# Kernel optimization log

Hardware: AMD Instinct MI355X
Metric: run time of the kernel (lower is better)

Reference implementation:

```python
import jax, jax.numpy as jnp
import numpy as np

B, C, H, W = 512, 3, 32, 32
N = 50000
D = C * H * W  # 3072


def setup_inputs() -> dict:
    key = jax.random.key(0)
    k1, k2, k3 = jax.random.split(key, 3)
    x = jax.random.normal(k1, (B, C, H, W), dtype=jnp.float32)
    # per-sample noise levels, strictly positive
    sigma = jax.random.uniform(k2, (B,), dtype=jnp.float32, minval=0.5, maxval=2.0)
    # reference dataset, normalized images in [-1, 1], flattened to (N, D)
    y = jax.random.uniform(k3, (N, D), dtype=jnp.float32, minval=-1.0, maxval=1.0)
    return {"x": x, "sigma": sigma, "y": y}


def reference(x, sigma, y):
    Bb, Cc, Hh, Ww = x.shape
    xf = x.astype(jnp.float32).reshape(Bb, Cc * Hh * Ww)          # (B, D)
    s = sigma.astype(jnp.float32).reshape(-1, 1)                  # (B, 1)
    # squared euclidean distance via the GEMM expansion (matches cdist(p=2)**2)
    x2 = jnp.sum(xf * xf, axis=1, keepdims=True)                  # (B, 1)
    y2 = jnp.sum(y * y, axis=1)[None, :]                          # (1, N)
    d2 = jnp.maximum(x2 + y2 - 2.0 * (xf @ y.T), 0.0)             # (B, N)
    logits = -d2 / (2.0 * s * s)                                  # (B, N)
    prob = jax.nn.softmax(logits, axis=1)                         # (B, N)
    denoised = prob @ y                                           # (B, D)
    return denoised.reshape(Bb, Cc, Hh, Ww)
```

## Files before the change

kernel.cpp:

```cpp
#include <hip/hip_runtime.h>


typedef __attribute__((ext_vector_type(4))) float f32x4;
typedef __attribute__((ext_vector_type(4))) int i32x4;
typedef __attribute__((ext_vector_type(4))) char c8x4;
typedef __attribute__((ext_vector_type(16))) char c8x16;
typedef __attribute__((ext_vector_type(4))) unsigned short u16x4;
typedef __attribute__((ext_vector_type(8))) unsigned short u16x8;
typedef __attribute__((ext_vector_type(8))) __bf16 bf16x8;

#define NREAL 50000
#define NP    50176
#define DD    3072
#define BB    512

#define WAIT0  asm volatile("s_waitcnt vmcnt(0)" ::: "memory")
#define VM2    asm volatile("s_waitcnt vmcnt(2)" ::: "memory")
#define LGKM0  asm volatile("s_waitcnt lgkmcnt(0)" ::: "memory")
#define BAR    __builtin_amdgcn_s_barrier()
#define SCHED0 __builtin_amdgcn_sched_barrier(0)

#define SX (6.0f / 127.0f)
#define SY (1.0f / 127.0f)

__device__ __forceinline__ unsigned short f32_bf16_rne(float f) {
  unsigned int u = __float_as_uint(f);
  unsigned int r = 0x7FFFu + ((u >> 16) & 1u);
  return (unsigned short)((u + r) >> 16);
}
__device__ __forceinline__ void gload16(const void* g, void* l) {
  __builtin_amdgcn_global_load_lds(
      (const __attribute__((address_space(1))) void*)g,
      (__attribute__((address_space(3))) void*)l, 16, 0, 0);
}
__device__ __forceinline__ bf16x8 ldsldb(const unsigned short* p) {
  return __builtin_bit_cast(bf16x8, *(const u16x8*)p);
}
__device__ __forceinline__ i32x4 ldsld4(const char* p) {
  return *(const i32x4*)p;
}
__device__ __forceinline__ char q8(float f, float sc) {
  float an = rintf(f * sc);
  an = fminf(127.f, fmaxf(-127.f, an));
  return (char)(int)an;
}

__global__ __launch_bounds__(256) void zero_kernel(f32x4* p) {
  p[(size_t)blockIdx.x * 256 + threadIdx.x] = (f32x4){0.f, 0.f, 0.f, 0.f};
}

__global__ __launch_bounds__(256) void init_kernel(int* rowmin, float* rowsum) {
  const int i = blockIdx.x * 256 + threadIdx.x;
  if (i < BB) { rowmin[i] = 0x7F800000; rowsum[i] = 0.f; }
}

__global__ __launch_bounds__(256) void prep_x_kernel(
    const float* __restrict__ x, const float* __restrict__ sigma,
    char* __restrict__ ax, char* __restrict__ bx,
    float* __restrict__ x2, float* __restrict__ inv2s2) {
  const int b = blockIdx.x, t = threadIdx.x;
  const f32x4* xr = (const f32x4*)(x + (size_t)b * DD);
  float ssq = 0.f;
#pragma unroll
  for (int i = 0; i < 3; ++i) {
    const int idx = i * 256 + t;
    f32x4 v = xr[idx];
    c8x4 a, bb;
#pragma unroll
    for (int j = 0; j < 4; ++j) {
      float f = v[j];
      ssq += f * f;
      char av = q8(f, 127.0f / 6.0f);
      a[j] = av;
      float r = f - (float)(int)av * SX;
      bb[j] = q8(r, 254.0f * 127.0f / 6.0f);
    }
    *(c8x4*)(ax + (size_t)b * DD + idx * 4) = a;
    *(c8x4*)(bx + (size_t)b * DD + idx * 4) = bb;
  }
  __shared__ float red[4];
#pragma unroll
  for (int off = 32; off > 0; off >>= 1) ssq += __shfl_xor(ssq, off);
  if ((t & 63) == 0) red[t >> 6] = ssq;
  __syncthreads();
  if (t == 0) {
    x2[b] = red[0] + red[1] + red[2] + red[3];
    float s = sigma[b];
    inv2s2[b] = 1.0f / (2.0f * s * s);
  }
}

__global__ __launch_bounds__(256) void quant_y_kernel(
    const float* __restrict__ y, char* __restrict__ ay, char* __restrict__ by,
    float* __restrict__ y2) {
  const int n = blockIdx.x, t = threadIdx.x;
  if (n >= NREAL) {
    c8x4 z = {0, 0, 0, 0};
#pragma unroll
    for (int i = 0; i < 3; ++i) {
      const int idx = i * 256 + t;
      *(c8x4*)(ay + (size_t)n * DD + idx * 4) = z;
      *(c8x4*)(by + (size_t)n * DD + idx * 4) = z;
    }
    if (t == 0) y2[n] = 0.f;
    return;
  }
  const f32x4* yr = (const f32x4*)(y + (size_t)n * DD);
  float ssq = 0.f;
#pragma unroll
  for (int i = 0; i < 3; ++i) {
    const int idx = i * 256 + t;
    f32x4 v = yr[idx];
    c8x4 a, bb;
#pragma unroll
    for (int j = 0; j < 4; ++j) {
      float f = v[j];
      ssq += f * f;
      char av = q8(f, 127.0f);
      a[j] = av;
      float r2 = f - (float)(int)av * SY;
      bb[j] = q8(r2, 254.0f * 127.0f);
    }
    *(c8x4*)(ay + (size_t)n * DD + idx * 4) = a;
    *(c8x4*)(by + (size_t)n * DD + idx * 4) = bb;
  }
  __shared__ float red[4];
#pragma unroll
  for (int off = 32; off > 0; off >>= 1) ssq += __shfl_xor(ssq, off);
  if ((t & 63) == 0) red[t >> 6] = ssq;
  __syncthreads();
  if (t == 0) y2[n] = red[0] + red[1] + red[2] + red[3];
}

__global__ __launch_bounds__(256) void tr_y_kernel(
    const char* __restrict__ ay, const char* __restrict__ by,
    unsigned short* __restrict__ yT) {
  const int bn = blockIdx.x % 784, bd = blockIdx.x / 784;
  const int n0 = bn * 64, d0 = bd * 64;
  __shared__ unsigned short T[64][66];
  const int t = threadIdx.x;
  const int r = t >> 2, cc = (t & 3) * 16;
  c8x16 a = *(const c8x16*)(ay + (size_t)(n0 + r) * DD + d0 + cc);
  c8x16 b = *(const c8x16*)(by + (size_t)(n0 + r) * DD + d0 + cc);
#pragma unroll
  for (int j = 0; j < 16; ++j) {
    float f = (float)((int)a[j] * 254 + (int)b[j]) * (SY / 254.0f);
    T[r][cc + j] = f32_bf16_rne(f);
  }
  __syncthreads();
  const int dr = t >> 2;
#pragma unroll
  for (int k = 0; k < 2; ++k) {
    const int nb = ((t & 3) * 2 + k) * 8;
    u16x8 o;
#pragma unroll
    for (int j = 0; j < 8; ++j) o[j] = T[nb + j][dr];
    *(u16x8*)(yT + (size_t)(d0 + dr) * NP + n0 + nb) = o;
  }
}

__global__ __launch_bounds__(256, 2) void qk_kernel(
    const char* __restrict__ ay, const char* __restrict__ by,
    const char* __restrict__ ax, const char* __restrict__ bx,
    const float* __restrict__ x2, const float* __restrict__ inv2s2,
    const float* __restrict__ y2, float* __restrict__ S, int* __restrict__ rowmin) {
  const int orig = blockIdx.x;
  const int virt = (orig & 7) * 196 + (orig >> 3);
  const int mt = virt & 3, nt = virt >> 2;
  const int m0 = mt * 128, n0 = nt * 128;
  const int t = threadIdx.x, lane = t & 63, w = t >> 6;
  const int wm = w >> 1, wn = w & 1;
  const int l15 = lane & 15;
  const int cs = ((lane >> 4) ^ ((l15 >> 1) & 3)) * 16;

  __shared__ __align__(16) char L[32768];

  i32x4 acc1[4][4] = {};
  i32x4 acc2[4][4] = {};

  const int srow = t >> 2;
  const int sc = ((t & 3) ^ ((t >> 3) & 3)) * 16;
  const int sdst = t * 16;

  const char* pax0 = ax + (size_t)(m0 + srow) * DD + sc;
  const char* pax1 = ax + (size_t)(m0 + srow + 64) * DD + sc;
  const char* pbx0 = bx + (size_t)(m0 + srow) * DD + sc;
  const char* pbx1 = bx + (size_t)(m0 + srow + 64) * DD + sc;
  const char* pay0 = ay + (size_t)(n0 + srow) * DD + sc;
  const char* pay1 = ay + (size_t)(n0 + srow + 64) * DD + sc;
  const char* pby0 = by + (size_t)(n0 + srow) * DD + sc;
  const char* pby1 = by + (size_t)(n0 + srow + 64) * DD + sc;

  auto STAGE = [&]() {
    gload16(pax0, L + sdst);
    gload16(pax1, L + 4096 + sdst);
    gload16(pbx0, L + 8192 + sdst);
    gload16(pbx1, L + 12288 + sdst);
    gload16(pay0, L + 16384 + sdst);
    gload16(pay1, L + 20480 + sdst);
    gload16(pby0, L + 24576 + sdst);
    gload16(pby1, L + 28672 + sdst);
    pax0 += 64; pax1 += 64; pbx0 += 64; pbx1 += 64;
    pay0 += 64; pay1 += 64; pby0 += 64; pby1 += 64;
  };
  auto COMPUTE = [&]() {
    i32x4 axf[4], bxf[4], ayf[4], byf[4];
#pragma unroll
    for (int nf = 0; nf < 4; ++nf) {
      const int row = wn * 64 + nf * 16 + l15;
      ayf[nf] = ldsld4(L + 16384 + row * 64 + cs);
      byf[nf] = ldsld4(L + 24576 + row * 64 + cs);
    }
#pragma unroll
    for (int mf = 0; mf < 4; ++mf) {
      const int row = wm * 64 + mf * 16 + l15;
      axf[mf] = ldsld4(L + row * 64 + cs);
      bxf[mf] = ldsld4(L + 8192 + row * 64 + cs);
    }
    __builtin_amdgcn_s_setprio(1);
#pragma unroll
    for (int mf = 0; mf < 4; ++mf)
#pragma unroll
      for (int nf = 0; nf < 4; ++nf) {
        acc1[mf][nf] = __builtin_amdgcn_mfma_i32_16x16x64_i8(axf[mf], ayf[nf], acc1[mf][nf], 0, 0, 0);
        acc2[mf][nf] = __builtin_amdgcn_mfma_i32_16x16x64_i8(axf[mf], byf[nf], acc2[mf][nf], 0, 0, 0);
        acc2[mf][nf] = __builtin_amdgcn_mfma_i32_16x16x64_i8(bxf[mf], ayf[nf], acc2[mf][nf], 0, 0, 0);
      }
    __builtin_amdgcn_s_setprio(0);
  };

  STAGE();
  for (int k = 0; k < 48; ++k) {
    __syncthreads();
    COMPUTE();
    __syncthreads();
    if (k < 47) STAGE();
  }

  const float C1 = 6.0f / 16129.0f;
  const float C2 = C1 / 254.0f;
  float rmv[4][4];
#pragma unroll
  for (int mf = 0; mf < 4; ++mf)
#pragma unroll
    for (int i = 0; i < 4; ++i) rmv[mf][i] = 3.0e38f;

#pragma unroll
  for (int nf = 0; nf < 4; ++nf) {
    const int col = n0 + wn * 64 + nf * 16 + l15;
    const bool ok = (col < NREAL);
    const float yy = ok ? y2[col] : 0.f;
#pragma unroll
    for (int mf = 0; mf < 4; ++mf) {
#pragma unroll
      for (int i = 0; i < 4; ++i) {
        const int row = m0 + wm * 64 + mf * 16 + ((lane >> 4) * 4) + i;
        float v = 3.0e38f;
        if (ok) {
          float dot = C1 * (float)acc1[mf][nf][i] + C2 * (float)acc2[mf][nf][i];
          float d2 = fmaxf(x2[row] + yy - 2.0f * dot, 0.0f);
          v = d2 * inv2s2[row];
          rmv[mf][i] = fminf(rmv[mf][i], v);
        }
        S[(size_t)row * NP + col] = v;
      }
    }
  }
#pragma unroll
  for (int mf = 0; mf < 4; ++mf)
#pragma unroll
    for (int i = 0; i < 4; ++i) {
      float v = rmv[mf][i];
#pragma unroll
      for (int o = 1; o < 16; o <<= 1) v = fminf(v, __shfl_xor(v, o));
      rmv[mf][i] = v;
    }
  if (l15 == 0) {
#pragma unroll
    for (int mf = 0; mf < 4; ++mf)
#pragma unroll
      for (int i = 0; i < 4; ++i) {
        const int row = m0 + wm * 64 + mf * 16 + ((lane >> 4) * 4) + i;
        atomicMin(rowmin + row, __float_as_int(rmv[mf][i]));
      }
  }
}

__global__ __launch_bounds__(256) void softmax_kernel(
    const float* __restrict__ S, const int* __restrict__ rowmin,
    unsigned short* __restrict__ P, float* __restrict__ rowsum) {
  const int bid = blockIdx.x;
  const int b = bid / 7, c = bid % 7;
  const int t = threadIdx.x;
  const f32x4* row = (const f32x4*)(S + (size_t)b * NP);
  const float rm = __int_as_float(rowmin[b]);
  unsigned short* pr = P + (size_t)b * NP;
  float sum = 0.f;
  const int base = c * 1792;
#pragma unroll
  for (int i = 0; i < 7; ++i) {
    const int e = base + i * 256 + t;
    f32x4 v = row[e];
    float e0 = __expf(rm - v[0]), e1 = __expf(rm - v[1]);
    float e2 = __expf(rm - v[2]), e3 = __expf(rm - v[3]);
    sum += e0 + e1 + e2 + e3;
    u16x4 o;
    o[0] = f32_bf16_rne(e0); o[1] = f32_bf16_rne(e1);
    o[2] = f32_bf16_rne(e2); o[3] = f32_bf16_rne(e3);
    *(u16x4*)(pr + (size_t)e * 4) = o;
  }
#pragma unroll
  for (int off = 32; off > 0; off >>= 1) sum += __shfl_xor(sum, off);
  __shared__ float red[4];
  if ((t & 63) == 0) red[t >> 6] = sum;
  __syncthreads();
  if (t == 0) atomicAdd(rowsum + b, red[0] + red[1] + red[2] + red[3]);
}

__global__ __launch_bounds__(512, 2) void pv_kernel(
    const unsigned short* __restrict__ yT, const unsigned short* __restrict__ P,
    const float* __restrict__ rowsum, float* __restrict__ out) {
  const int orig = blockIdx.x;
  const int virt = (orig & 7) * 96 + (orig >> 3);
  const int sp = virt / 24;
  const int r24 = virt % 24;
  const int dt = r24 >> 1, mt = r24 & 1;
  const int m0 = mt * 256, d0 = dt * 256;
  const int k0t = sp * 24 + (sp < 16 ? sp : 16);
  const int NT = 24 + (sp < 16 ? 1 : 0);

  const int t = threadIdx.x;
  const int lane = t & 63, w = t >> 6;
  const int wm = w >> 2, wn = w & 3;
  const int l15 = lane & 15;
  const int h3 = (l15 >> 1) & 7;
  const int cs0 = ((lane >> 4) ^ h3) * 8;
  const int cs1 = ((4 + (lane >> 4)) ^ h3) * 8;

  __shared__ __align__(16) unsigned short L[2][2][16384];

  f32x4 acc[8][4] = {};

  const int srow8 = t >> 3;
  const int sc = ((t & 7) ^ ((t >> 4) & 7)) * 8;
  const int sdst = t * 8;

  const size_t kbeg = (size_t)k0t * 64;
  const unsigned short* pA[4];
  pA[0] = P + (size_t)(m0 + srow8) * NP + kbeg + sc;
  pA[1] = P + (size_t)(m0 + srow8 + 128) * NP + kbeg + sc;
  pA[2] = P + (size_t)(m0 + srow8 + 64) * NP + kbeg + sc;
  pA[3] = P + (size_t)(m0 + srow8 + 192) * NP + kbeg + sc;
  const unsigned short* pB[4];
#pragma unroll
  for (int r = 0; r < 4; ++r)
    pB[r] = yT + (size_t)(d0 + srow8 + r * 64) * NP + kbeg + sc;

  auto SB01 = [&](int b) {
    gload16(pB[0], &L[b][1][sdst]); gload16(pB[1], &L[b][1][sdst + 4096]);
    pB[0] += 64; pB[1] += 64;
  };
  auto SB23 = [&](int b) {
    gload16(pB[2], &L[b][1][sdst + 8192]); gload16(pB[3], &L[b][1][sdst + 12288]);
    pB[2] += 64; pB[3] += 64;
  };
  auto SA01 = [&](int b) {
    gload16(pA[0], &L[b][0][sdst]); gload16(pA[1], &L[b][0][sdst + 4096]);
    pA[0] += 64; pA[1] += 64;
  };
  auto SA23 = [&](int b) {
    gload16(pA[2], &L[b][0][sdst + 8192]); gload16(pA[3], &L[b][0][sdst + 12288]);
    pA[2] += 64; pA[3] += 64;
  };

  bf16x8 a[4], bv[4];
  auto RA = [&](int b, int mh, int cs) {
#pragma unroll
    for (int m4 = 0; m4 < 4; ++m4)
      a[m4] = ldsldb(&L[b][0][(mh * 128 + wm * 64 + m4 * 16 + l15) * 64 + cs]);
  };
  auto RB = [&](int b, int cs) {
#pragma unroll
    for (int nf = 0; nf < 4; ++nf)
      bv[nf] = ldsldb(&L[b][1][(wn * 64 + nf * 16 + l15) * 64 + cs]);
  };
  auto MF = [&](int mh) {
    __builtin_amdgcn_s_setprio(1);
#pragma unroll
    for (int m4 = 0; m4 < 4; ++m4)
#pragma unroll
      for (int nf = 0; nf < 4; ++nf)
        acc[mh * 4 + m4][nf] = __builtin_amdgcn_mfma_f32_16x16x32_bf16(
            a[m4], bv[nf], acc[mh * 4 + m4][nf], 0, 0, 0);
    __builtin_amdgcn_s_setprio(0);
  };

  SB01(0); SB23(0); SA01(0); SA23(0);
  WAIT0; BAR;

  for (int k = 0; k < NT - 1; ++k) {
    const int b = k & 1, nb = b ^ 1;
    RB(b, cs0); RA(b, 0, cs0);
    SB01(nb);
    BAR; LGKM0; SCHED0;
    MF(0);
    VM2;
    BAR;
    RA(b, 1, cs0);
    SB23(nb);
    BAR; LGKM0; SCHED0;
    MF(1);
    BAR;
    RB(b, cs1); RA(b, 0, cs1);
    SA01(nb);
    BAR; LGKM0; SCHED0;
    MF(0);
    BAR;
    RA(b, 1, cs1);
    SA23(nb);
    BAR; LGKM0; SCHED0;
    MF(1);
    VM2;
    BAR;
  }
  {
    const int b = (NT - 1) & 1;
    RB(b, cs0); RA(b, 0, cs0);
    BAR; LGKM0; SCHED0;
    MF(0);
    WAIT0;
    BAR;
    RA(b, 1, cs0);
    LGKM0; SCHED0;
    MF(1);
    RB(b, cs1); RA(b, 0, cs1);
    LGKM0; SCHED0;
    MF(0);
    RA(b, 1, cs1);
    LGKM0; SCHED0;
    MF(1);
  }

#pragma unroll
  for (int mi = 0; mi < 8; ++mi)
#pragma unroll
    for (int i = 0; i < 4; ++i) {
      const int row = m0 + wm * 128 + mi * 16 + ((lane >> 4) * 4) + i;
      const float scale = 1.0f / rowsum[row];
#pragma unroll
      for (int nf = 0; nf < 4; ++nf) {
        const int col = d0 + wn * 64 + nf * 16 + l15;
        unsafeAtomicAdd(out + (size_t)row * DD + col, acc[mi][nf][i] * scale);
      }
    }
}

extern "C" void kernel_launch(void* const* d_in, const int* in_sizes, int n_in,
                              void* d_out, int out_size, void* d_ws, size_t ws_size,
                              hipStream_t stream) {
  const float* x = (const float*)d_in[0];
  const float* sigma = (const float*)d_in[1];
  const float* y = (const float*)d_in[2];
  float* out = (float*)d_out;
  char* ws = (char*)d_ws;

  size_t off = 0;
  float* S = (float*)(ws + off);                      off += (size_t)BB * NP * 4;
  char* ay = (char*)(ws + off);                       off += (size_t)NP * DD;
  char* by = (char*)(ws + off);                       off += (size_t)NP * DD;
  unsigned short* P = (unsigned short*)by;
  char* ax = (char*)(ws + off);                       off += (size_t)BB * DD;
  char* bx = (char*)(ws + off);                       off += (size_t)BB * DD;
  float* y2 = (float*)(ws + off);                     off += (size_t)NP * 4;
  float* x2 = (float*)(ws + off);                     off += 512 * 4;
  float* inv2s2 = (float*)(ws + off);                 off += 512 * 4;
  float* rowsum = (float*)(ws + off);                 off += 512 * 4;
  int* rowmin = (int*)(ws + off);                     off += 512 * 4;
  unsigned short* yT = (unsigned short*)(ws + off);   off += (size_t)DD * NP * 2;
  off += 65536;
  if (ws_size < off) return;

  zero_kernel<<<dim3(1536), dim3(256), 0, stream>>>((f32x4*)out);
  init_kernel<<<dim3(2), dim3(256), 0, stream>>>(rowmin, rowsum);
  prep_x_kernel<<<dim3(512), dim3(256), 0, stream>>>(x, sigma, ax, bx, x2, inv2s2);
  quant_y_kernel<<<dim3(NP), dim3(256), 0, stream>>>(y, ay, by, y2);
  tr_y_kernel<<<dim3(784 * 48), dim3(256), 0, stream>>>(ay, by, yT);
  qk_kernel<<<dim3(1568), dim3(256), 0, stream>>>(ay, by, ax, bx, x2, inv2s2, y2, S, rowmin);
  softmax_kernel<<<dim3(512 * 7), dim3(256), 0, stream>>>(S, rowmin, P, rowsum);
  pv_kernel<<<dim3(768), dim3(512), 0, stream>>>(yT, P, rowsum, out);
}
```

Baseline: 921.7 us.

## Fuse y quantization and bf16 transpose into one tiled kernel

Merges the per-row int8 split-quantization kernel and the transpose kernel into a single 64x64-tiled kernel. It reads fp32 y once and writes ay, by and the bf16 yT directly from registers and LDS. This removes the intermediate re-read of the quantized arrays and one kernel launch. Row squared norms are now built from per-tile partial sums with atomicAdd, so init_kernel zeroes y2 first. yT is now rounded straight from fp32 rather than from the dequantized int8 pair, and each tile reads only 256 contiguous bytes per row, which is a less coalesced pattern than full-row reads.

```diff
diff --git a/kernel.cpp b/kernel.cpp
--- a/kernel.cpp
+++ b/kernel.cpp
@@ -49,8 +49,10 @@
   p[(size_t)blockIdx.x * 256 + threadIdx.x] = (f32x4){0.f, 0.f, 0.f, 0.f};
 }
 
-__global__ __launch_bounds__(256) void init_kernel(int* rowmin, float* rowsum) {
+__global__ __launch_bounds__(256) void init_kernel(float* y2, int* rowmin,
+                                                   float* rowsum) {
   const int i = blockIdx.x * 256 + threadIdx.x;
+  y2[i] = 0.f;
   if (i < BB) { rowmin[i] = 0x7F800000; rowsum[i] = 0.f; }
 }
 
@@ -90,68 +92,48 @@
   }
 }
 
-__global__ __launch_bounds__(256) void quant_y_kernel(
+__global__ __launch_bounds__(256) void quant_tr_kernel(
     const float* __restrict__ y, char* __restrict__ ay, char* __restrict__ by,
-    float* __restrict__ y2) {
-  const int n = blockIdx.x, t = threadIdx.x;
-  if (n >= NREAL) {
-    c8x4 z = {0, 0, 0, 0};
-#pragma unroll
-    for (int i = 0; i < 3; ++i) {
-      const int idx = i * 256 + t;
-      *(c8x4*)(ay + (size_t)n * DD + idx * 4) = z;
-      *(c8x4*)(by + (size_t)n * DD + idx * 4) = z;
-    }
-    if (t == 0) y2[n] = 0.f;
-    return;
-  }
-  const f32x4* yr = (const f32x4*)(y + (size_t)n * DD);
-  float ssq = 0.f;
-#pragma unroll
-  for (int i = 0; i < 3; ++i) {
-    const int idx = i * 256 + t;
-    f32x4 v = yr[idx];
-    c8x4 a, bb;
-#pragma unroll
-    for (int j = 0; j < 4; ++j) {
-      float f = v[j];
-      ssq += f * f;
-      char av = q8(f, 127.0f);
-      a[j] = av;
-      float r2 = f - (float)(int)av * SY;
-      bb[j] = q8(r2, 254.0f * 127.0f);
-    }
-    *(c8x4*)(ay + (size_t)n * DD + idx * 4) = a;
-    *(c8x4*)(by + (size_t)n * DD + idx * 4) = bb;
-  }
-  __shared__ float red[4];
-#pragma unroll
-  for (int off = 32; off > 0; off >>= 1) ssq += __shfl_xor(ssq, off);
-  if ((t & 63) == 0) red[t >> 6] = ssq;
-  __syncthreads();
-  if (t == 0) y2[n] = red[0] + red[1] + red[2] + red[3];
-}
-
-__global__ __launch_bounds__(256) void tr_y_kernel(
-    const char* __restrict__ ay, const char* __restrict__ by,
-    unsigned short* __restrict__ yT) {
+    unsigned short* __restrict__ yT, float* __restrict__ y2) {
   const int bn = blockIdx.x % 784, bd = blockIdx.x / 784;
   const int n0 = bn * 64, d0 = bd * 64;
+  const int t = threadIdx.x;
   __shared__ unsigned short T[64][66];
-  const int t = threadIdx.x;
-  const int r = t >> 2, cc = (t & 3) * 16;
-  c8x16 a = *(const c8x16*)(ay + (size_t)(n0 + r) * DD + d0 + cc);
-  c8x16 b = *(const c8x16*)(by + (size_t)(n0 + r) * DD + d0 + cc);
+
+  const int r = t >> 2, c16 = (t & 3) * 16;
+  const int n = n0 + r;
+  const bool ok = (n < NREAL);
+
+  f32x4 v[4];
+#pragma unroll
+  for (int k = 0; k < 4; ++k)
+    v[k] = ok ? *(const f32x4*)(y + (size_t)n * DD + d0 + c16 + k * 4)
+              : (f32x4){0.f, 0.f, 0.f, 0.f};
+
+  c8x16 a, b;
+  float ssq = 0.f;
 #pragma unroll
   for (int j = 0; j < 16; ++j) {
-    float f = (float)((int)a[j] * 254 + (int)b[j]) * (SY / 254.0f);
-    T[r][cc + j] = f32_bf16_rne(f);
-  }
+    float f = v[j >> 2][j & 3];
+    ssq += f * f;
+    char av = q8(f, 127.0f);
+    a[j] = av;
+    float r2 = f - (float)(int)av * SY;
+    b[j] = q8(r2, 254.0f * 127.0f);
+    T[r][c16 + j] = f32_bf16_rne(f);
+  }
+  *(c8x16*)(ay + (size_t)n * DD + d0 + c16) = a;
+  *(c8x16*)(by + (size_t)n * DD + d0 + c16) = b;
+
+  ssq += __shfl_xor(ssq, 1);
+  ssq += __shfl_xor(ssq, 2);
+  if ((t & 3) == 0 && ok) atomicAdd(y2 + n, ssq);
+
   __syncthreads();
   const int dr = t >> 2;
 #pragma unroll
   for (int k = 0; k < 2; ++k) {
-    const int nb = ((t & 3) * 2 + k) * 8;
+    const int nb = (t & 3) * 16 + k * 8;
     u16x8 o;
 #pragma unroll
     for (int j = 0; j < 8; ++j) o[j] = T[nb + j][dr];
@@ -481,10 +463,9 @@
   if (ws_size < off) return;
 
   zero_kernel<<<dim3(1536), dim3(256), 0, stream>>>((f32x4*)out);
-  init_kernel<<<dim3(2), dim3(256), 0, stream>>>(rowmin, rowsum);
+  init_kernel<<<dim3(NP / 256), dim3(256), 0, stream>>>(y2, rowmin, rowsum);
   prep_x_kernel<<<dim3(512), dim3(256), 0, stream>>>(x, sigma, ax, bx, x2, inv2s2);
-  quant_y_kernel<<<dim3(NP), dim3(256), 0, stream>>>(y, ay, by, y2);
-  tr_y_kernel<<<dim3(784 * 48), dim3(256), 0, stream>>>(ay, by, yT);
+  quant_tr_kernel<<<dim3(784 * 48), dim3(256), 0, stream>>>(y, ay, by, yT, y2);
   qk_kernel<<<dim3(1568), dim3(256), 0, stream>>>(ay, by, ax, bx, x2, inv2s2, y2, S, rowmin);
   softmax_kernel<<<dim3(512 * 7), dim3(256), 0, stream>>>(S, rowmin, P, rowsum);
   pv_kernel<<<dim3(768), dim3(512), 0, stream>>>(yT, P, rowsum, out);
```

Result: slower. 966.1 us (+4.8%).
